# Kernel tuning notes

Hardware: AMD Instinct MI355X
Metric: run time of the kernel (lower is better)

Reference implementation:

```python
import jax, jax.numpy as jnp
import numpy as np

B, C, H, W = 4, 5, 96, 96


def setup_inputs() -> dict:
    key = jax.random.key(0)
    ks = jax.random.split(key, 5)
    x = jax.random.normal(ks[0], (B, C, H, W), dtype=jnp.float32)
    wq = jax.random.normal(ks[1], (C, C), dtype=jnp.float32) * 0.1  # 1x1 conv weight [out,in]
    bq = jax.random.normal(ks[2], (C,), dtype=jnp.float32) * 0.1
    wk = jax.random.normal(ks[3], (C, C), dtype=jnp.float32) * 0.1
    bk = jax.random.normal(ks[4], (C,), dtype=jnp.float32) * 0.1
    return {"x": x, "wq": wq, "bq": bq, "wk": wk, "bk": bk}


def reference(x, wq, bq, wk, bk):
    b, c, h, w = x.shape
    n = h * w
    # 1x1 convs == per-pixel linear maps over channels
    q = jnp.einsum('bchw,oc->bohw', x, wq) + bq[None, :, None, None]
    k = jnp.einsum('bchw,oc->bohw', x, wk) + bk[None, :, None, None]
    proj_query = q.reshape(b, c, n).transpose(0, 2, 1)  # [B, N, C]
    proj_key = k.reshape(b, c, n)                        # [B, C, N]
    energy = jnp.einsum('bnc,bcm->bnm', proj_query, proj_key)  # [B, N, N], no scaling
    attention = jax.nn.softmax(energy, axis=-1)
    return attention
```

## Files before the change

### kernel.cpp

```cpp
#include <hip/hip_runtime.h>

constexpr int B_ = 4, C_ = 5, H_ = 96, W_ = 96;
constexpr int N_ = H_ * W_;
constexpr int NPT = N_ / 256;
constexpr int NJ = NPT / 4;

typedef float    f32x4 __attribute__((ext_vector_type(4)));
typedef _Float16 f16x4 __attribute__((ext_vector_type(4)));

__global__ __launch_bounds__(256) void proj_qk(
    const float* __restrict__ x,
    const float* __restrict__ wq, const float* __restrict__ bq,
    const float* __restrict__ wk, const float* __restrict__ bk,
    float* __restrict__ q, _Float16* __restrict__ k)
{
    int idx = blockIdx.x * 256 + threadIdx.x;
    if (idx >= B_ * N_) return;
    int b = idx / N_;
    int n = idx - b * N_;
    float xi[C_];
#pragma unroll
    for (int i = 0; i < C_; ++i) xi[i] = x[(size_t)(b * C_ + i) * N_ + n];
#pragma unroll
    for (int c = 0; c < C_; ++c) {
        float aq = bq[c], ak = bk[c];
#pragma unroll
        for (int i = 0; i < C_; ++i) {
            aq = fmaf(wq[c * C_ + i], xi[i], aq);
            ak = fmaf(wk[c * C_ + i], xi[i], ak);
        }
        q[(size_t)(b * C_ + c) * N_ + n] = aq;
        k[(size_t)(b * C_ + c) * N_ + n] = (_Float16)ak;
    }
}

__global__ __launch_bounds__(256) void attn_row(
    const float* __restrict__ q, const _Float16* __restrict__ k,
    float* __restrict__ out)
{
    const int row = blockIdx.x;
    const int b = row / N_;
    const int n = row - b * N_;
    const int tid = threadIdx.x;

    float qv[C_];
#pragma unroll
    for (int c = 0; c < C_; ++c) qv[c] = q[(size_t)(b * C_ + c) * N_ + n];

    const _Float16* kb = k + (size_t)b * C_ * N_;

    f32x4 e[NJ];
    float lsum = 0.f;
#pragma unroll
    for (int j = 0; j < NJ; ++j) {
        const int m4 = (j * 256 + tid) * 4;
        f32x4 acc = {0.f, 0.f, 0.f, 0.f};
#pragma unroll
        for (int c = 0; c < C_; ++c) {
            const f16x4 kh = *reinterpret_cast<const f16x4*>(kb + (size_t)c * N_ + m4);
            acc.x = fmaf(qv[c], (float)kh.x, acc.x);
            acc.y = fmaf(qv[c], (float)kh.y, acc.y);
            acc.z = fmaf(qv[c], (float)kh.z, acc.z);
            acc.w = fmaf(qv[c], (float)kh.w, acc.w);
        }
        acc.x = __expf(acc.x);
        acc.y = __expf(acc.y);
        acc.z = __expf(acc.z);
        acc.w = __expf(acc.w);
        e[j] = acc;
        lsum += (acc.x + acc.y) + (acc.z + acc.w);
    }

    __shared__ float redsum[4];

#pragma unroll
    for (int off = 32; off >= 1; off >>= 1)
        lsum += __shfl_xor(lsum, off, 64);
    const int wv = tid >> 6;
    if ((tid & 63) == 0) redsum[wv] = lsum;
    __syncthreads();
    const float inv = 1.f / ((redsum[0] + redsum[1]) + (redsum[2] + redsum[3]));

    float* orow = out + (size_t)row * N_;
#pragma unroll
    for (int j = 0; j < NJ; ++j) {
        const int m4 = (j * 256 + tid) * 4;
        f32x4 o;
        o.x = e[j].x * inv;
        o.y = e[j].y * inv;
        o.z = e[j].z * inv;
        o.w = e[j].w * inv;
        __builtin_nontemporal_store(o, reinterpret_cast<f32x4*>(orow + m4));
    }
}

extern "C" void kernel_launch(void* const* d_in, const int* in_sizes, int n_in,
                              void* d_out, int out_size, void* d_ws, size_t ws_size,
                              hipStream_t stream)
{
    const float* x  = (const float*)d_in[0];
    const float* wq = (const float*)d_in[1];
    const float* bq = (const float*)d_in[2];
    const float* wk = (const float*)d_in[3];
    const float* bk = (const float*)d_in[4];
    float* out = (float*)d_out;

    float*    q = (float*)d_ws;
    _Float16* k = (_Float16*)(q + (size_t)B_ * C_ * N_);

    proj_qk<<<(B_ * N_ + 255) / 256, 256, 0, stream>>>(x, wq, bq, wk, bk, q, k);
    attn_row<<<B_ * N_, 256, 0, stream>>>(q, k, out);
}
```

Measured before the change: 262.9 us.

## Use persistent blocks that cache K in LDS and process many rows

Replaces the one-block-per-row attention kernel with 256 persistent 512-thread blocks. Each block loads the batch's fp16 K matrix into shared memory once, then loops over 144 rows, two rows at a time. This removes repeated global/L2 reads of K and per-row launch overhead. In exchange it uses about 92 KB of LDS per block, which limits occupancy, and adds a block barrier each iteration.

```diff
diff --git a/kernel.cpp b/kernel.cpp
--- a/kernel.cpp
+++ b/kernel.cpp
@@ -2,8 +2,7 @@
 
 constexpr int B_ = 4, C_ = 5, H_ = 96, W_ = 96;
 constexpr int N_ = H_ * W_;
-constexpr int NPT = N_ / 256;
-constexpr int NJ = NPT / 4;
+constexpr int NJ = 9;
 
 typedef float    f32x4 __attribute__((ext_vector_type(4)));
 typedef _Float16 f16x4 __attribute__((ext_vector_type(4)));
@@ -34,63 +33,83 @@
     }
 }
 
-__global__ __launch_bounds__(256) void attn_row(
+__global__ __launch_bounds__(512) void attn_persist(
     const float* __restrict__ q, const _Float16* __restrict__ k,
     float* __restrict__ out)
 {
-    const int row = blockIdx.x;
-    const int b = row / N_;
-    const int n = row - b * N_;
-    const int tid = threadIdx.x;
+    __shared__ _Float16 klds[C_ * N_];
+    __shared__ float    redsum[2][8];
 
-    float qv[C_];
+    const int bid  = blockIdx.x;
+    const int b    = bid >> 6;
+    const int rg   = bid & 63;
+    const int tid  = threadIdx.x;
+
+    {
+        const uint* __restrict__ src =
+            reinterpret_cast<const uint*>(k + (size_t)b * C_ * N_);
+        uint* dst = reinterpret_cast<uint*>(klds);
 #pragma unroll
-    for (int c = 0; c < C_; ++c) qv[c] = q[(size_t)(b * C_ + c) * N_ + n];
+        for (int i = 0; i < (C_ * N_ / 2) / 512; ++i)
+            dst[i * 512 + tid] = src[i * 512 + tid];
+    }
+    __syncthreads();
 
-    const _Float16* kb = k + (size_t)b * C_ * N_;
+    const int half = tid >> 8;
+    const int tidh = tid & 255;
+    const int wv   = tid >> 6;
 
-    f32x4 e[NJ];
-    float lsum = 0.f;
+    const int nbase = rg * 144;
+    for (int it = 0; it < 72; ++it) {
+        const int n = nbase + it * 2 + half;
+
+        float qv[C_];
 #pragma unroll
-    for (int j = 0; j < NJ; ++j) {
-        const int m4 = (j * 256 + tid) * 4;
-        f32x4 acc = {0.f, 0.f, 0.f, 0.f};
+        for (int c = 0; c < C_; ++c)
+            qv[c] = q[(size_t)(b * C_ + c) * N_ + n];
+
+        f32x4 e[NJ];
+        float lsum = 0.f;
 #pragma unroll
-        for (int c = 0; c < C_; ++c) {
-            const f16x4 kh = *reinterpret_cast<const f16x4*>(kb + (size_t)c * N_ + m4);
-            acc.x = fmaf(qv[c], (float)kh.x, acc.x);
-            acc.y = fmaf(qv[c], (float)kh.y, acc.y);
-            acc.z = fmaf(qv[c], (float)kh.z, acc.z);
-            acc.w = fmaf(qv[c], (float)kh.w, acc.w);
+        for (int j = 0; j < NJ; ++j) {
+            const int m4 = (j * 256 + tidh) * 4;
+            f32x4 acc = {0.f, 0.f, 0.f, 0.f};
+#pragma unroll
+            for (int c = 0; c < C_; ++c) {
+                const f16x4 kh =
+                    *reinterpret_cast<const f16x4*>(klds + c * N_ + m4);
+                acc.x = fmaf(qv[c], (float)kh.x, acc.x);
+                acc.y = fmaf(qv[c], (float)kh.y, acc.y);
+                acc.z = fmaf(qv[c], (float)kh.z, acc.z);
+                acc.w = fmaf(qv[c], (float)kh.w, acc.w);
+            }
+            acc.x = __expf(acc.x);
+            acc.y = __expf(acc.y);
+            acc.z = __expf(acc.z);
+            acc.w = __expf(acc.w);
+            e[j] = acc;
+            lsum += (acc.x + acc.y) + (acc.z + acc.w);
         }
-        acc.x = __expf(acc.x);
-        acc.y = __expf(acc.y);
-        acc.z = __expf(acc.z);
-        acc.w = __expf(acc.w);
-        e[j] = acc;
-        lsum += (acc.x + acc.y) + (acc.z + acc.w);
-    }
-
-    __shared__ float redsum[4];
 
 #pragma unroll
-    for (int off = 32; off >= 1; off >>= 1)
-        lsum += __shfl_xor(lsum, off, 64);
-    const int wv = tid >> 6;
-    if ((tid & 63) == 0) redsum[wv] = lsum;
-    __syncthreads();
-    const float inv = 1.f / ((redsum[0] + redsum[1]) + (redsum[2] + redsum[3]));
+        for (int off = 32; off >= 1; off >>= 1)
+            lsum += __shfl_xor(lsum, off, 64);
+        if ((tid & 63) == 0) redsum[it & 1][wv] = lsum;
+        __syncthreads();
+        const float* rs = redsum[it & 1] + half * 4;
+        const float inv = 1.f / ((rs[0] + rs[1]) + (rs[2] + rs[3]));
 
-    float* orow = out + (size_t)row * N_;
+        float* orow = out + (size_t)(b * N_ + n) * N_;
 #pragma unroll
-    for (int j = 0; j < NJ; ++j) {
-        const int m4 = (j * 256 + tid) * 4;
-        f32x4 o;
-        o.x = e[j].x * inv;
-        o.y = e[j].y * inv;
-        o.z = e[j].z * inv;
-        o.w = e[j].w * inv;
-        __builtin_nontemporal_store(o, reinterpret_cast<f32x4*>(orow + m4));
+        for (int j = 0; j < NJ; ++j) {
+            const int m4 = (j * 256 + tidh) * 4;
+            f32x4 o;
+            o.x = e[j].x * inv;
+            o.y = e[j].y * inv;
+            o.z = e[j].z * inv;
+            o.w = e[j].w * inv;
+            __builtin_nontemporal_store(o, reinterpret_cast<f32x4*>(orow + m4));
+        }
     }
 }
 
@@ -109,5 +128,5 @@
     _Float16* k = (_Float16*)(q + (size_t)B_ * C_ * N_);
 
     proj_qk<<<(B_ * N_ + 255) / 256, 256, 0, stream>>>(x, wq, bq, wk, bk, q, k);
-    attn_row<<<B_ * N_, 256, 0, stream>>>(q, k, out);
+    attn_persist<<<256, 512, 0, stream>>>(q, k, out);
 }
```

New measurement: 284.4 us. 8.2% more time.

## Process four rows per block with two-pass recompute instead of register caching

Applied to the files above, without the earlier changes.

Each block now handles four query rows, so every loaded K vector is reused across four rows. Exponentials are no longer held in registers between the sum and the normalisation; a second pass reloads K and recomputes the energies and exps. This cuts K loads per row and block count, at the cost of doing the exp and FMA work twice. The output is ~1.36 GB of fp32 writes, so the kernel is likely store-bandwidth bound and the extra compute may stay hidden.

```diff
diff --git a/kernel.cpp b/kernel.cpp
--- a/kernel.cpp
+++ b/kernel.cpp
@@ -2,8 +2,8 @@
 
 constexpr int B_ = 4, C_ = 5, H_ = 96, W_ = 96;
 constexpr int N_ = H_ * W_;
-constexpr int NPT = N_ / 256;
-constexpr int NJ = NPT / 4;
+constexpr int NJ = 9;
+constexpr int R_ = 4;
 
 typedef float    f32x4 __attribute__((ext_vector_type(4)));
 typedef _Float16 f16x4 __attribute__((ext_vector_type(4)));
@@ -34,63 +34,90 @@
     }
 }
 
-__global__ __launch_bounds__(256) void attn_row(
+__global__ __launch_bounds__(256) void attn_rows2p(
     const float* __restrict__ q, const _Float16* __restrict__ k,
     float* __restrict__ out)
 {
-    const int row = blockIdx.x;
-    const int b = row / N_;
-    const int n = row - b * N_;
+    constexpr int BPB = N_ / R_;
+    const int g   = blockIdx.x;
+    const int b   = g / BPB;
+    const int n0  = (g - b * BPB) * R_;
     const int tid = threadIdx.x;
+    const int wv  = tid >> 6;
 
-    float qv[C_];
+    float qv[R_][C_];
 #pragma unroll
-    for (int c = 0; c < C_; ++c) qv[c] = q[(size_t)(b * C_ + c) * N_ + n];
+    for (int r = 0; r < R_; ++r)
+#pragma unroll
+        for (int c = 0; c < C_; ++c)
+            qv[r][c] = q[(size_t)(b * C_ + c) * N_ + (n0 + r)];
 
     const _Float16* kb = k + (size_t)b * C_ * N_;
 
-    f32x4 e[NJ];
-    float lsum = 0.f;
+    float lsum[R_] = {0.f, 0.f, 0.f, 0.f};
 #pragma unroll
     for (int j = 0; j < NJ; ++j) {
         const int m4 = (j * 256 + tid) * 4;
-        f32x4 acc = {0.f, 0.f, 0.f, 0.f};
+        f16x4 kh[C_];
 #pragma unroll
-        for (int c = 0; c < C_; ++c) {
-            const f16x4 kh = *reinterpret_cast<const f16x4*>(kb + (size_t)c * N_ + m4);
-            acc.x = fmaf(qv[c], (float)kh.x, acc.x);
-            acc.y = fmaf(qv[c], (float)kh.y, acc.y);
-            acc.z = fmaf(qv[c], (float)kh.z, acc.z);
-            acc.w = fmaf(qv[c], (float)kh.w, acc.w);
+        for (int c = 0; c < C_; ++c)
+            kh[c] = *reinterpret_cast<const f16x4*>(kb + (size_t)c * N_ + m4);
+#pragma unroll
+        for (int r = 0; r < R_; ++r) {
+            f32x4 acc = {0.f, 0.f, 0.f, 0.f};
+#pragma unroll
+            for (int c = 0; c < C_; ++c) {
+                acc.x = fmaf(qv[r][c], (float)kh[c].x, acc.x);
+                acc.y = fmaf(qv[r][c], (float)kh[c].y, acc.y);
+                acc.z = fmaf(qv[r][c], (float)kh[c].z, acc.z);
+                acc.w = fmaf(qv[r][c], (float)kh[c].w, acc.w);
+            }
+            lsum[r] += (__expf(acc.x) + __expf(acc.y)) +
+                       (__expf(acc.z) + __expf(acc.w));
         }
-        acc.x = __expf(acc.x);
-        acc.y = __expf(acc.y);
-        acc.z = __expf(acc.z);
-        acc.w = __expf(acc.w);
-        e[j] = acc;
-        lsum += (acc.x + acc.y) + (acc.z + acc.w);
     }
 
-    __shared__ float redsum[4];
+    __shared__ float redsum[R_][4];
+#pragma unroll
+    for (int r = 0; r < R_; ++r) {
+        float s = lsum[r];
+#pragma unroll
+        for (int off = 32; off >= 1; off >>= 1)
+            s += __shfl_xor(s, off, 64);
+        if ((tid & 63) == 0) redsum[r][wv] = s;
+    }
+    __syncthreads();
+    float inv[R_];
+#pragma unroll
+    for (int r = 0; r < R_; ++r)
+        inv[r] = 1.f / ((redsum[r][0] + redsum[r][1]) +
+                        (redsum[r][2] + redsum[r][3]));
 
-#pragma unroll
-    for (int off = 32; off >= 1; off >>= 1)
-        lsum += __shfl_xor(lsum, off, 64);
-    const int wv = tid >> 6;
-    if ((tid & 63) == 0) redsum[wv] = lsum;
-    __syncthreads();
-    const float inv = 1.f / ((redsum[0] + redsum[1]) + (redsum[2] + redsum[3]));
-
-    float* orow = out + (size_t)row * N_;
 #pragma unroll
     for (int j = 0; j < NJ; ++j) {
         const int m4 = (j * 256 + tid) * 4;
-        f32x4 o;
-        o.x = e[j].x * inv;
-        o.y = e[j].y * inv;
-        o.z = e[j].z * inv;
-        o.w = e[j].w * inv;
-        __builtin_nontemporal_store(o, reinterpret_cast<f32x4*>(orow + m4));
+        f16x4 kh[C_];
+#pragma unroll
+        for (int c = 0; c < C_; ++c)
+            kh[c] = *reinterpret_cast<const f16x4*>(kb + (size_t)c * N_ + m4);
+#pragma unroll
+        for (int r = 0; r < R_; ++r) {
+            f32x4 acc = {0.f, 0.f, 0.f, 0.f};
+#pragma unroll
+            for (int c = 0; c < C_; ++c) {
+                acc.x = fmaf(qv[r][c], (float)kh[c].x, acc.x);
+                acc.y = fmaf(qv[r][c], (float)kh[c].y, acc.y);
+                acc.z = fmaf(qv[r][c], (float)kh[c].z, acc.z);
+                acc.w = fmaf(qv[r][c], (float)kh[c].w, acc.w);
+            }
+            f32x4 o;
+            o.x = __expf(acc.x) * inv[r];
+            o.y = __expf(acc.y) * inv[r];
+            o.z = __expf(acc.z) * inv[r];
+            o.w = __expf(acc.w) * inv[r];
+            __builtin_nontemporal_store(
+                o, reinterpret_cast<f32x4*>(out + (size_t)(b * N_ + n0 + r) * N_ + m4));
+        }
     }
 }
 
@@ -109,5 +136,5 @@
     _Float16* k = (_Float16*)(q + (size_t)B_ * C_ * N_);
 
     proj_qk<<<(B_ * N_ + 255) / 256, 256, 0, stream>>>(x, wq, bq, wk, bk, q, k);
-    attn_row<<<B_ * N_, 256, 0, stream>>>(q, k, out);
+    attn_rows2p<<<B_ * (N_ / R_), 256, 0, stream>>>(q, k, out);
 }
```

Result: faster. 256.4 us, median of 2 (-2.5%).
